# Optimization experiments

Measured on AMD Instinct MI355X. Metric: run time of the kernel, lower is better.

Reference implementation:

```python
import jax, jax.numpy as jnp
import numpy as np
import math


def _conv(x, w, scale, bias, stride=1):
    # Ultralytics-style Conv: Conv2d(bias=False, pad=k//2) + BatchNorm (folded into
    # per-channel scale/bias) + SiLU
    k = w.shape[-1]
    p = k // 2
    y = jax.lax.conv_general_dilated(x, w, (stride, stride), [(p, p), (p, p)],
                                     dimension_numbers=('NCHW', 'OIHW', 'NCHW'))
    y = y * scale[None, :, None, None] + bias[None, :, None, None]
    return y * jax.nn.sigmoid(y)


def setup_inputs() -> dict:
    key = jax.random.key(0)
    ks = jax.random.split(key, 24)
    B, CH1, CH2, H1, W1, HW = 32, 512, 512, 20, 20, 40
    EMB = 256
    s = 0.05
    half = CH1 // 2
    d = {}
    d['x1'] = jax.random.normal(ks[0], (B, CH1, H1, W1), jnp.float32)
    d['x2'] = jax.random.normal(ks[1], (B, CH2, HW, HW), jnp.float32)
    # CrossAttention params
    d['q_w'] = jax.random.normal(ks[2], (EMB, CH1, 3, 3)) * s
    d['q_s'] = 1.0 + jax.random.normal(ks[3], (EMB,)) * s
    d['q_b'] = jax.random.normal(ks[4], (EMB,)) * s
    d['key_w'] = jax.random.normal(ks[5], (EMB, CH2)) * s
    # MGFAB / CSHA params (CA = channel-MLP sigmoid gate, rate=4)
    d['ca_w1'] = jax.random.normal(ks[6], (half // 4, half)) * s
    d['ca_b1'] = jnp.zeros((half // 4,))
    d['ca_w2'] = jax.random.normal(ks[7], (half, half // 4)) * s
    d['ca_b2'] = jnp.zeros((half,))
    d['sa1_w'] = jax.random.normal(ks[8], (half, half, 3, 3)) * s
    d['sa1_s'] = 1.0 + jax.random.normal(ks[9], (half,)) * s
    d['sa1_b'] = jax.random.normal(ks[10], (half,)) * s
    d['sa2_w'] = jax.random.normal(ks[11], (half, half, 3, 3)) * s
    d['sa2_s'] = 1.0 + jax.random.normal(ks[12], (half,)) * s
    d['sa2_b'] = jax.random.normal(ks[13], (half,)) * s
    d['conv2_w'] = jax.random.normal(ks[14], (CH1, 3 * half, 1, 1)) * s
    d['conv2_s'] = 1.0 + jax.random.normal(ks[15], (CH1,)) * s
    d['conv2_b'] = jax.random.normal(ks[16], (CH1,)) * s
    # conv3 branch (single Conv since patch_size[0] < 5)
    d['c3_w'] = jax.random.normal(ks[17], (CH2, CH2, 3, 3)) * s
    d['c3_s'] = 1.0 + jax.random.normal(ks[18], (CH2,)) * s
    d['c3_b'] = jax.random.normal(ks[19], (CH2,)) * s
    return d


def _forward(x1, x2, q_w, q_s, q_b, key_w, ca_w1, ca_b1, ca_w2, ca_b2,
             sa1_w, sa1_s, sa1_b, sa2_w, sa2_s, sa2_b,
             conv2_w, conv2_s, conv2_b, c3_w, c3_s, c3_b):
    NH, PH, PW = 8, 4, 4
    b, c, h, w = x2.shape
    cH = c // NH                       # channels per head
    nph, npw = h // PH, w // PW        # patch grid
    L = nph * npw                      # number of patches == number of q tokens

    # ---- CrossAttention ----
    # value: per-head flattened patches [b*NH, L, cH*PH*PW] (row-major over h,w)
    v = x2.reshape(b * NH, cH, nph, PH, npw, PW).transpose(0, 2, 4, 1, 3, 5)
    v = v.reshape(b * NH, L, cH * PH * PW)
    # key: avg-pool each patch -> linear(c -> emb) -> split heads
    kp = x2.reshape(b, c, nph, PH, npw, PW).mean(axis=(3, 5))  # [b, c, nph, npw]
    k = jnp.einsum('bcl,ec->ble', kp.reshape(b, c, L), key_w)  # [b, L, EMB]
    dh = k.shape[-1] // NH
    k = k.reshape(b, L, NH, dh).transpose(0, 2, 1, 3).reshape(b * NH, L, dh)
    # query: stride-2 conv on x1 -> tokens -> split heads
    q = _conv(x1, q_w, q_s, q_b, stride=2)                     # [b, EMB, nph, npw]
    q = q.reshape(b, -1, L).transpose(0, 2, 1)                 # [b, L, EMB]
    q = q.reshape(b, L, NH, dh).transpose(0, 2, 1, 3).reshape(b * NH, L, dh)
    score = jnp.einsum('nqd,nkd->nqk', q, k) / math.sqrt(dh)
    wts = jax.nn.softmax(score, axis=-1)                       # dropout = identity (eval)
    y = jnp.einsum('nqk,nkv->nqv', wts, v)                     # [b*NH, L, cH*PH*PW]
    # reassemble patches back into [b, c, h, w]
    attn = y.reshape(b, NH, nph, npw, cH, PH, PW).transpose(0, 1, 4, 2, 5, 3, 6)
    attn = attn.reshape(b, c, h, w)

    # ---- conv3 branch with residual ----
    x2_out = _conv(attn, c3_w, c3_s, c3_b) + attn

    x1_up = jnp.repeat(jnp.repeat(x1, 2, axis=2), 2, axis=3)   # [b, ch1, h, w]
    half = x1_up.shape[1] // 2
    a0, a1 = x1_up[:, :half], x1_up[:, half:]
    # CA: channel MLP gate
    xp = a1.transpose(0, 2, 3, 1)                              # [b, h, w, half]
    att = jnp.maximum(xp @ ca_w1.T + ca_b1, 0.0) @ ca_w2.T + ca_b2
    x_ca = a1 * jax.nn.sigmoid(att.transpose(0, 3, 1, 2))
    # SA: two 3x3 Convs + residual
    x_sa = _conv(_conv(x_ca, sa1_w, sa1_s, sa1_b), sa2_w, sa2_s, sa2_b)
    a2 = x_sa + x_ca
    cat = jnp.concatenate([a0, a1, a2], axis=1)                # [b, 3*half, h, w]
    x1_out = _conv(cat, conv2_w, conv2_s, conv2_b)             # [b, ch1, h, w]

    return jnp.concatenate([x1_out, x2_out], axis=1)           # [b, ch1+ch2, h, w]


def reference(x1, x2, q_w, q_s, q_b, key_w, ca_w1, ca_b1, ca_w2, ca_b2,
              sa1_w, sa1_s, sa1_b, sa2_w, sa2_s, sa2_b,
              conv2_w, conv2_s, conv2_b, c3_w, c3_s, c3_b):
    return _forward(x1, x2, q_w, q_s, q_b, key_w, ca_w1, ca_b1, ca_w2, ca_b2,
                    sa1_w, sa1_s, sa1_b, sa2_w, sa2_s, sa2_b,
                    conv2_w, conv2_s, conv2_b, c3_w, c3_s, c3_b)
```

## Files before the change

kernel.cpp:

```cpp
#include <hip/hip_runtime.h>
#include <hip/hip_bf16.h>

using bf16 = __hip_bfloat16;
using bf16x2 = __hip_bfloat162;
typedef __attribute__((ext_vector_type(8))) short short8;
typedef __attribute__((ext_vector_type(4))) float f32x4;

__device__ __forceinline__ float b2f(bf16 v) { return __bfloat162float(v); }
__device__ __forceinline__ bf16 f2b(float v) { return __float2bfloat16(v); }

__device__ __forceinline__ void gload_lds16(const bf16* g, bf16* l)
{
    __builtin_amdgcn_global_load_lds(
        (const __attribute__((address_space(1))) void*)g,
        (__attribute__((address_space(3))) void*)l,
        16, 0, 0);
}

__global__ __launch_bounds__(256) void nchw_to_nhwc(const float* __restrict__ in,
                                                    bf16* __restrict__ out,
                                                    int C, int H, int W, int pad)
{
    __shared__ bf16 tile[64][68];
    const int S = H * W;
    const int HP = H + 2 * pad, WP = W + 2 * pad;
    const int b = blockIdx.x, s0 = blockIdx.y * 64, c0 = blockIdx.z * 64;
    const int t = threadIdx.x;
    const int a = t & 63, q = t >> 6;
#pragma unroll
    for (int i = 0; i < 16; ++i) {
        int cl = q + i * 4;
        int s = s0 + a;
        tile[cl][a] = (s < S) ? f2b(in[((size_t)b * C + c0 + cl) * S + s]) : f2b(0.f);
    }
    __syncthreads();
#pragma unroll
    for (int i = 0; i < 16; ++i) {
        int sl = q + i * 4;
        int s = s0 + sl;
        if (s < S) {
            int y = s / W, x = s - (s / W) * W;
            out[(((size_t)b * HP + y + pad) * WP + x + pad) * C + c0 + a] = tile[a][sl];
        }
    }
}

__global__ __launch_bounds__(256) void halo_zero(bf16* __restrict__ buf, int W, int C)
{
    const int b = blockIdx.x, y = blockIdx.y;
    const int P = W + 2;
    const bf16 z = f2b(0.f);
    bf16* row = buf + ((size_t)b * P + y) * P * C;
    if (y == 0 || y == P - 1) {
        for (int i = threadIdx.x; i < P * C; i += 256) row[i] = z;
    } else {
        for (int i = threadIdx.x; i < 2 * C; i += 256) {
            const int x = (i < C) ? 0 : P - 1;
            const int c = (i < C) ? i : i - C;
            row[(size_t)x * C + c] = z;
        }
    }
}

__global__ __launch_bounds__(256) void pack_out(const bf16* __restrict__ x1o,
                                                const bf16* __restrict__ x2o,
                                                float* __restrict__ out)
{
    __shared__ bf16 tile[64][68];
    const int b = blockIdx.x, s0 = blockIdx.y * 64, ch0 = blockIdx.z * 64;
    const bf16* src = (ch0 < 512) ? x1o : x2o;
    const int c0 = ch0 & 511;
    const int t = threadIdx.x;
    const int a = t & 63, q = t >> 6;
#pragma unroll
    for (int i = 0; i < 16; ++i) {
        int sl = q + i * 4;
        tile[sl][a] = src[((size_t)b * 1600 + s0 + sl) * 512 + c0 + a];
    }
    __syncthreads();
#pragma unroll
    for (int i = 0; i < 16; ++i) {
        int cl = q + i * 4;
        out[((size_t)b * 1024 + ch0 + cl) * 1600 + s0 + a] = b2f(tile[a][cl]);
    }
}

__global__ __launch_bounds__(256) void reorder_w(const float* __restrict__ w,
                                                 bf16* __restrict__ wr,
                                                 int C, int total)
{
    int i = blockIdx.x * 256 + threadIdx.x;
    if (i >= total) return;
    int nineC = 9 * C;
    int o = i / nineC;
    int r = i - o * nineC;
    int tap = r / C;
    int c = r - tap * C;
    wr[i] = f2b(w[((size_t)o * C + c) * 9 + tap]);
}

__global__ __launch_bounds__(256) void f32_to_bf16(const float* __restrict__ in,
                                                   bf16* __restrict__ out, int n)
{
    int i = blockIdx.x * 256 + threadIdx.x;
    if (i < n) out[i] = f2b(in[i]);
}

__global__ __launch_bounds__(256) void pool_kp(const bf16* __restrict__ x2n,
                                               bf16* __restrict__ kp)
{
    const int p = blockIdx.x;
    const int b = p / 100, l = p - (p / 100) * 100;
    const int ph = l / 10, pw = l - (l / 10) * 10;
    const int t = threadIdx.x;
    const bf16x2* base = (const bf16x2*)(x2n + (((size_t)(b * 40 + ph * 4) * 40) + pw * 4) * 512) + t;
    float sx = 0.f, sy = 0.f;
#pragma unroll
    for (int py = 0; py < 4; ++py)
#pragma unroll
        for (int px = 0; px < 4; ++px) {
            float2 v = __bfloat1622float2(base[(py * 40 + px) * 256]);
            sx += v.x; sy += v.y;
        }
    ((bf16x2*)(kp + (size_t)p * 512))[t] = __float22bfloat162_rn(make_float2(sx * 0.0625f, sy * 0.0625f));
}

__global__ __launch_bounds__(256) void ca_mlp(const bf16* __restrict__ x1n,
                                              const float* __restrict__ w1, const float* __restrict__ b1,
                                              const float* __restrict__ w2, const float* __restrict__ b2,
                                              bf16* __restrict__ xca)
{
    __shared__ float a1v[256];
    __shared__ float part[4][64];
    __shared__ float hid[64];
    const int blk = blockIdx.x;
    const int b = blk / 400;
    const int rem = blk - b * 400;
    const int y = rem / 20, x = rem - (rem / 20) * 20;
    const int t = threadIdx.x;
    const bf16* src = x1n + ((size_t)(b * 22 + y + 1) * 22 + x + 1) * 512 + 256;
    a1v[t] = b2f(src[t]);
    __syncthreads();
    {
        const int h = t & 63, seg = t >> 6;
        float acc = 0.f;
        const float* wp = w1 + (size_t)h * 256 + seg * 64;
        const float* ap = a1v + seg * 64;
#pragma unroll 8
        for (int c = 0; c < 64; ++c) acc += wp[c] * ap[c];
        part[seg][h] = acc;
    }
    __syncthreads();
    if (t < 64)
        hid[t] = fmaxf(part[0][t] + part[1][t] + part[2][t] + part[3][t] + b1[t], 0.f);
    __syncthreads();
    float acc2 = b2[t];
    const float* w2p = w2 + (size_t)t * 64;
#pragma unroll 8
    for (int h = 0; h < 64; ++h) acc2 += w2p[h] * hid[h];
    const float g = 1.f / (1.f + __expf(-acc2));
    const bf16 o = f2b(a1v[t] * g);
    const size_t obase = ((size_t)(b * 42 + 2 * y + 1) * 42 + 2 * x + 1) * 256 + t;
    xca[obase] = o;
    xca[obase + 256] = o;
    xca[obase + 42 * 256] = o;
    xca[obase + 42 * 256 + 256] = o;
}

__global__ __launch_bounds__(256, 1)
void attn_kernel(const float* __restrict__ q, const float* __restrict__ k,
                 const bf16* __restrict__ x2n, bf16* __restrict__ attn)
{
    __shared__ float sc[100][100];
    __shared__ bf16 wT[100][104];
    const int t = threadIdx.x;
    const int n = blockIdx.x;
    const int b = n >> 3, hd = n & 7;
    const float* qn = q + (size_t)n * 3200;
    const float* kn = k + (size_t)n * 3200;
    for (int e = t; e < 10000; e += 256) {
        const int i = e / 100;
        const int j = e - i * 100;
        const float4* qa = (const float4*)(qn + i * 32);
        const float4* ka = (const float4*)(kn + j * 32);
        float d = 0.f;
#pragma unroll
        for (int u = 0; u < 8; ++u) {
            float4 xv = qa[u], yv = ka[u];
            d += xv.x * yv.x + xv.y * yv.y + xv.z * yv.z + xv.w * yv.w;
        }
        sc[i][j] = d * 0.17677669529663687f;
    }
    __syncthreads();
    if (t < 100) {
        float mx = -1e30f;
        for (int j = 0; j < 100; ++j) mx = fmaxf(mx, sc[t][j]);
        float s = 0.f;
        for (int j = 0; j < 100; ++j) s += __expf(sc[t][j] - mx);
        const float inv = 1.f / s;
        for (int j = 0; j < 100; ++j) wT[j][t] = f2b(__expf(sc[t][j] - mx) * inv);
    }
    __syncthreads();
    const int ch0 = (t & 15) * 4;
    const int pix = t >> 4;
    const int py = pix >> 2, px = pix & 3;
    const bf16* vbase = x2n + (((size_t)(b * 40 + py) * 40) + px) * 512 + hd * 64 + ch0;
    for (int ql0 = 0; ql0 < 100; ql0 += 20) {
        float2 a0[20], a1[20];
#pragma unroll
        for (int i = 0; i < 20; ++i) { a0[i] = make_float2(0.f, 0.f); a1[i] = make_float2(0.f, 0.f); }
        for (int l = 0; l < 100; ++l) {
            const int ph = l / 10, pw = l - (l / 10) * 10;
            const bf16* vp = vbase + ((size_t)(ph * 160 + pw * 4)) * 512;
            const float2 v01 = __bfloat1622float2(*(const bf16x2*)vp);
            const float2 v23 = __bfloat1622float2(*(const bf16x2*)(vp + 2));
            const bf16x2* wp = (const bf16x2*)&wT[l][ql0];
#pragma unroll
            for (int ii = 0; ii < 10; ++ii) {
                const float2 w2 = __bfloat1622float2(wp[ii]);
                a0[ii * 2 + 0].x += w2.x * v01.x; a0[ii * 2 + 0].y += w2.x * v01.y;
                a1[ii * 2 + 0].x += w2.x * v23.x; a1[ii * 2 + 0].y += w2.x * v23.y;
                a0[ii * 2 + 1].x += w2.y * v01.x; a0[ii * 2 + 1].y += w2.y * v01.y;
                a1[ii * 2 + 1].x += w2.y * v23.x; a1[ii * 2 + 1].y += w2.y * v23.y;
            }
        }
#pragma unroll
        for (int i = 0; i < 20; ++i) {
            const int ql = ql0 + i;
            const int ph = ql / 10, pw = ql - (ql / 10) * 10;
            bf16* op = attn + (((size_t)(b * 42 + ph * 4 + py + 1) * 42) + pw * 4 + px + 1) * 512 + hd * 64 + ch0;
            *(bf16x2*)op = __float22bfloat162_rn(a0[i]);
            *(bf16x2*)(op + 2) = __float22bfloat162_rn(a1[i]);
        }
    }
}

enum ConvMode { M_QCONV = 0, M_SA1 = 1, M_SA2 = 2, M_C3 = 3, M_CONV2 = 4, M_KPROJ = 5 };

template <int MODE>
__global__ __launch_bounds__(256, 2)
void conv_mfma(const bf16* __restrict__ in, const bf16* __restrict__ in2,
               const bf16* __restrict__ wr,
               const float* __restrict__ scale, const float* __restrict__ bias,
               const bf16* __restrict__ resid,
               bf16* __restrict__ outb, float* __restrict__ outf)
{
    constexpr int CIN  = (MODE == M_QCONV || MODE == M_C3 || MODE == M_KPROJ) ? 512
                       : (MODE == M_CONV2 ? 768 : 256);
    constexpr int TAPS = (MODE == M_CONV2 || MODE == M_KPROJ) ? 1 : 9;
    constexpr int SP   = (MODE == M_QCONV || MODE == M_KPROJ) ? 100 : 1600;
    constexpr int STR  = (MODE == M_QCONV) ? 2 : 1;
    constexpr int HP   = (MODE == M_QCONV) ? 22 : 42;
    constexpr int WOUT = (MODE == M_QCONV || MODE == M_KPROJ) ? 10 : 40;
    constexpr int K    = TAPS * CIN;
    constexpr int KD   = (TAPS == 9) ? 3 : 1;

    __shared__ bf16 Al[128][64];
    __shared__ bf16 Bl[128][64];

    const int t = threadIdx.x;
    const int p0 = blockIdx.x * 128;
    const int n0 = blockIdx.y * 128;

    int s_row[4], s_dst8[4], s_src8[4], s_b[4], s_oy[4], s_ox[4];
    const bf16* bB[4];
#pragma unroll
    for (int i = 0; i < 4; ++i) {
        const int task = t + i * 256;
        const int row = task >> 3, chk = task & 7;
        s_row[i] = row;
        s_dst8[i] = chk * 8;
        s_src8[i] = (chk ^ (row & 7)) * 8;
        const int p = p0 + row;
        const int bb = p / SP;
        const int s = p - bb * SP;
        s_b[i] = bb;
        s_oy[i] = s / WOUT;
        s_ox[i] = s - s_oy[i] * WOUT;
        bB[i] = wr + (size_t)(n0 + row) * K + s_src8[i];
    }

    const bf16* aP1[4];
    const bf16* aP2[4];
    if (MODE == M_CONV2) {
#pragma unroll
        for (int i = 0; i < 4; ++i) {
            aP1[i] = in + ((size_t)(s_b[i] * 22 + (s_oy[i] >> 1) + 1) * 22 + (s_ox[i] >> 1) + 1) * 512 + s_src8[i];
            aP2[i] = in2 + ((size_t)(s_b[i] * 1600 + s_oy[i] * 40 + s_ox[i])) * 256 + s_src8[i];
        }
    }
    if (MODE == M_KPROJ) {
#pragma unroll
        for (int i = 0; i < 4; ++i)
            aP1[i] = in + (size_t)(p0 + s_row[i]) * 512 + s_src8[i];
    }

    const int lane = t & 63;
    const int wv = t >> 6;
    const int m_off = (wv >> 1) * 64;
    const int n_off = (wv & 1) * 64;
    const int fr = lane & 15;
    const int qd = lane >> 4;
    const int xa = (fr & 7) << 4;

    f32x4 acc[4][4];
#pragma unroll
    for (int mi = 0; mi < 4; ++mi)
#pragma unroll
        for (int ni = 0; ni < 4; ++ni)
            acc[mi][ni] = (f32x4){0.f, 0.f, 0.f, 0.f};

    for (int ky = 0; ky < KD; ++ky)
    for (int kx = 0; kx < KD; ++kx) {
        const bf16* aT[4];
        if (TAPS == 9) {
#pragma unroll
            for (int i = 0; i < 4; ++i)
                aT[i] = in + ((size_t)((s_b[i] * HP + s_oy[i] * STR + ky) * HP) + s_ox[i] * STR + kx) * CIN + s_src8[i];
        }
        const int kk0 = (ky * KD + kx) * CIN;
        for (int c0 = 0; c0 < CIN; c0 += 64) {
#pragma unroll
            for (int i = 0; i < 4; ++i) {
                const bf16* sa;
                if (MODE == M_CONV2)      sa = (c0 < 512) ? (aP1[i] + c0) : (aP2[i] + (c0 - 512));
                else if (MODE == M_KPROJ) sa = aP1[i] + c0;
                else                      sa = aT[i] + c0;
                gload_lds16(sa, &Al[s_row[i]][s_dst8[i]]);
            }
#pragma unroll
            for (int i = 0; i < 4; ++i)
                gload_lds16(bB[i] + (kk0 + c0), &Bl[s_row[i]][s_dst8[i]]);
            __syncthreads();
#pragma unroll
            for (int ks = 0; ks < 2; ++ks) {
                short8 af[4], bfr[4];
                const int coff = (ks * 64 + qd * 16) ^ xa;
#pragma unroll
                for (int mi = 0; mi < 4; ++mi)
                    af[mi] = *(const short8*)((const char*)&Al[m_off + mi * 16 + fr][0] + coff);
#pragma unroll
                for (int ni = 0; ni < 4; ++ni)
                    bfr[ni] = *(const short8*)((const char*)&Bl[n_off + ni * 16 + fr][0] + coff);
#pragma unroll
                for (int mi = 0; mi < 4; ++mi)
#pragma unroll
                    for (int ni = 0; ni < 4; ++ni)
                        acc[mi][ni] = __builtin_amdgcn_mfma_f32_16x16x32_bf16(af[mi], bfr[ni], acc[mi][ni], 0, 0, 0);
            }
            __syncthreads();
        }
    }

#pragma unroll
    for (int ni = 0; ni < 4; ++ni) {
        const int nn = n0 + n_off + ni * 16 + fr;
        float scv = 1.f, bsv = 0.f;
        if (MODE != M_KPROJ) { scv = scale[nn]; bsv = bias[nn]; }
#pragma unroll
        for (int mi = 0; mi < 4; ++mi) {
            const int mb = p0 + m_off + mi * 16 + qd * 4;
#pragma unroll
            for (int r = 0; r < 4; ++r) {
                const int p = mb + r;
                const float v = acc[mi][ni][r];
                if (MODE == M_KPROJ) {
                    const int bb = p / 100, l = p - (p / 100) * 100;
                    outf[(((size_t)(bb * 8 + (nn >> 5))) * 100 + l) * 32 + (nn & 31)] = v;
                } else {
                    const float y = v * scv + bsv;
                    const float a = y / (1.f + __expf(-y));
                    if (MODE == M_QCONV) {
                        const int bb = p / 100, l = p - (p / 100) * 100;
                        outf[(((size_t)(bb * 8 + (nn >> 5))) * 100 + l) * 32 + (nn & 31)] = a;
                    } else if (MODE == M_SA1) {
                        const int bb = p / 1600; const int s = p - bb * 1600;
                        const int oy = s / 40, ox = s - (s / 40) * 40;
                        outb[(((size_t)(bb * 42 + oy + 1)) * 42 + ox + 1) * 256 + nn] = f2b(a);
                    } else if (MODE == M_SA2) {
                        const int bb = p / 1600; const int s = p - bb * 1600;
                        const int oy = s / 40, ox = s - (s / 40) * 40;
                        const size_t roff = (((size_t)(bb * 42 + oy + 1)) * 42 + ox + 1) * 256 + nn;
                        outb[(size_t)p * 256 + nn] = f2b(a + b2f(resid[roff]));
                    } else if (MODE == M_C3) {
                        const int bb = p / 1600; const int s = p - bb * 1600;
                        const int oy = s / 40, ox = s - (s / 40) * 40;
                        const size_t roff = (((size_t)(bb * 42 + oy + 1)) * 42 + ox + 1) * 512 + nn;
                        outb[(size_t)p * 512 + nn] = f2b(a + b2f(resid[roff]));
                    } else {
                        outb[(size_t)p * 512 + nn] = f2b(a);
                    }
                }
            }
        }
    }
}

extern "C" void kernel_launch(void* const* d_in, const int* in_sizes, int n_in,
                              void* d_out, int out_size, void* d_ws, size_t ws_size,
                              hipStream_t stream)
{
    const float* x1      = (const float*)d_in[0];
    const float* x2      = (const float*)d_in[1];
    const float* q_w     = (const float*)d_in[2];
    const float* q_s     = (const float*)d_in[3];
    const float* q_b     = (const float*)d_in[4];
    const float* key_w   = (const float*)d_in[5];
    const float* ca_w1   = (const float*)d_in[6];
    const float* ca_b1   = (const float*)d_in[7];
    const float* ca_w2   = (const float*)d_in[8];
    const float* ca_b2   = (const float*)d_in[9];
    const float* sa1_w   = (const float*)d_in[10];
    const float* sa1_s   = (const float*)d_in[11];
    const float* sa1_b   = (const float*)d_in[12];
    const float* sa2_w   = (const float*)d_in[13];
    const float* sa2_s   = (const float*)d_in[14];
    const float* sa2_b   = (const float*)d_in[15];
    const float* conv2_w = (const float*)d_in[16];
    const float* conv2_s = (const float*)d_in[17];
    const float* conv2_b = (const float*)d_in[18];
    const float* c3_w    = (const float*)d_in[19];
    const float* c3_s    = (const float*)d_in[20];
    const float* c3_b    = (const float*)d_in[21];

    char* ws = (char*)d_ws;
    const size_t o_x1n  = 0;
    const size_t o_x2n  = 15859712;
    const size_t o_attn = 68288512;
    const size_t o_xca  = 126091264;
    const size_t o_tbuf = 154992640;
    const size_t o_a2   = 183894016;
    const size_t o_ws1  = 210108416;
    const size_t o_ws2  = 211288064;
    const size_t o_wc2  = 212467712;
    const size_t o_k    = o_tbuf;
    const size_t o_q    = o_tbuf + 3276800;
    const size_t o_wkey = o_tbuf + 6553600;
    const size_t o_kp   = o_a2;
    const size_t o_wq   = o_a2 + 3276800;
    const size_t o_wc3  = o_xca;

    bf16*  x1n    = (bf16*)(ws + o_x1n);
    bf16*  x2n    = (bf16*)(ws + o_x2n);
    float* k_attn = (float*)(ws + o_k);
    float* q_attn = (float*)(ws + o_q);
    bf16*  attn   = (bf16*)(ws + o_attn);
    bf16*  xca    = (bf16*)(ws + o_xca);
    bf16*  tbuf   = (bf16*)(ws + o_tbuf);
    bf16*  a2     = (bf16*)(ws + o_a2);
    bf16*  wq     = (bf16*)(ws + o_wq);
    bf16*  wc3    = (bf16*)(ws + o_wc3);
    bf16*  wsa1   = (bf16*)(ws + o_ws1);
    bf16*  wsa2   = (bf16*)(ws + o_ws2);
    bf16*  kp     = (bf16*)(ws + o_kp);
    bf16*  wkey   = (bf16*)(ws + o_wkey);
    bf16*  wc2    = (bf16*)(ws + o_wc2);
    bf16*  x2o    = (bf16*)(ws + o_x2n);
    bf16*  x1o    = (bf16*)(ws + o_attn);

    const dim3 blk(256);

    halo_zero<<<dim3(32, 22), blk, 0, stream>>>(x1n, 20, 512);
    halo_zero<<<dim3(32, 42), blk, 0, stream>>>(xca, 40, 256);
    halo_zero<<<dim3(32, 42), blk, 0, stream>>>(attn, 40, 512);

    nchw_to_nhwc<<<dim3(32, 7, 8), blk, 0, stream>>>(x1, x1n, 512, 20, 20, 1);
    nchw_to_nhwc<<<dim3(32, 25, 8), blk, 0, stream>>>(x2, x2n, 512, 40, 40, 0);
    reorder_w<<<4608, blk, 0, stream>>>(q_w,  wq,   512, 256 * 512 * 9);
    reorder_w<<<2304, blk, 0, stream>>>(sa1_w, wsa1, 256, 256 * 256 * 9);
    reorder_w<<<2304, blk, 0, stream>>>(sa2_w, wsa2, 256, 256 * 256 * 9);
    f32_to_bf16<<<512, blk, 0, stream>>>(key_w, wkey, 256 * 512);
    f32_to_bf16<<<1536, blk, 0, stream>>>(conv2_w, wc2, 512 * 768);
    pool_kp<<<3200, blk, 0, stream>>>(x2n, kp);

    conv_mfma<M_KPROJ><<<dim3(25, 2), blk, 0, stream>>>(kp, nullptr, wkey,
        nullptr, nullptr, nullptr, nullptr, k_attn);
    conv_mfma<M_QCONV><<<dim3(25, 2), blk, 0, stream>>>(x1n, nullptr, wq,
        q_s, q_b, nullptr, nullptr, q_attn);

    attn_kernel<<<256, blk, 0, stream>>>(q_attn, k_attn, x2n, attn);

    halo_zero<<<dim3(32, 42), blk, 0, stream>>>(tbuf, 40, 256);

    ca_mlp<<<12800, blk, 0, stream>>>(x1n, ca_w1, ca_b1, ca_w2, ca_b2, xca);

    conv_mfma<M_SA1><<<dim3(400, 2), blk, 0, stream>>>(xca, nullptr, wsa1,
        sa1_s, sa1_b, nullptr, tbuf, nullptr);
    conv_mfma<M_SA2><<<dim3(400, 2), blk, 0, stream>>>(tbuf, nullptr, wsa2,
        sa2_s, sa2_b, xca, a2, nullptr);

    reorder_w<<<9216, blk, 0, stream>>>(c3_w, wc3, 512, 512 * 512 * 9);
    conv_mfma<M_C3><<<dim3(400, 4), blk, 0, stream>>>(attn, nullptr, wc3,
        c3_s, c3_b, attn, x2o, nullptr);
    conv_mfma<M_CONV2><<<dim3(400, 4), blk, 0, stream>>>(x1n, a2, wc2,
        conv2_s, conv2_b, nullptr, x1o, nullptr);

    pack_out<<<dim3(32, 25, 16), blk, 0, stream>>>(x1o, x2o, (float*)d_out);

    (void)in_sizes; (void)n_in; (void)out_size; (void)ws_size;
}
```

Before: 1.464 ms.

## Add double-buffered 256x256-tile MFMA conv kernel for large convolutions

Adds a new 512-thread implicit-GEMM conv kernel with 256x256 output tiles and double-buffered LDS. It prefetches the next K-slice with direct global-to-LDS loads interleaved between MFMA phases, using explicit barriers and s_setprio. The SA1, SA2, C3 and CONV2 convolutions now use it, and the old kernel is trimmed to the small Q-conv and key-projection cases. Larger tiles raise operand reuse and the overlap hides load latency, but LDS use grows to 128KB per block. The SA convs now launch only 200 blocks, which may underfill the GPU.

```diff
diff --git a/kernel.cpp b/kernel.cpp
--- a/kernel.cpp
+++ b/kernel.cpp
@@ -16,6 +16,10 @@
         (__attribute__((address_space(3))) void*)l,
         16, 0, 0);
 }
+
+#define PH_BAR() do { __builtin_amdgcn_sched_barrier(0); __builtin_amdgcn_s_barrier(); __builtin_amdgcn_sched_barrier(0); } while (0)
+#define WAIT_LGKM0() do { asm volatile("s_waitcnt lgkmcnt(0)" ::: "memory"); __builtin_amdgcn_sched_barrier(0); } while (0)
+#define WAIT_VM0() do { asm volatile("s_waitcnt vmcnt(0)" ::: "memory"); __builtin_amdgcn_sched_barrier(0); } while (0)
 
 __global__ __launch_bounds__(256) void nchw_to_nhwc(const float* __restrict__ in,
                                                     bf16* __restrict__ out,
@@ -239,19 +243,15 @@
 
 template <int MODE>
 __global__ __launch_bounds__(256, 2)
-void conv_mfma(const bf16* __restrict__ in, const bf16* __restrict__ in2,
-               const bf16* __restrict__ wr,
+void conv_mfma(const bf16* __restrict__ in, const bf16* __restrict__ wr,
                const float* __restrict__ scale, const float* __restrict__ bias,
-               const bf16* __restrict__ resid,
-               bf16* __restrict__ outb, float* __restrict__ outf)
-{
-    constexpr int CIN  = (MODE == M_QCONV || MODE == M_C3 || MODE == M_KPROJ) ? 512
-                       : (MODE == M_CONV2 ? 768 : 256);
-    constexpr int TAPS = (MODE == M_CONV2 || MODE == M_KPROJ) ? 1 : 9;
-    constexpr int SP   = (MODE == M_QCONV || MODE == M_KPROJ) ? 100 : 1600;
-    constexpr int STR  = (MODE == M_QCONV) ? 2 : 1;
-    constexpr int HP   = (MODE == M_QCONV) ? 22 : 42;
-    constexpr int WOUT = (MODE == M_QCONV || MODE == M_KPROJ) ? 10 : 40;
+               float* __restrict__ outf)
+{
+    constexpr int CIN  = 512;
+    constexpr int TAPS = (MODE == M_KPROJ) ? 1 : 9;
+    constexpr int STR  = 2;
+    constexpr int HP   = 22;
+    constexpr int WOUT = 10;
     constexpr int K    = TAPS * CIN;
     constexpr int KD   = (TAPS == 9) ? 3 : 1;
 
@@ -272,8 +272,8 @@
         s_dst8[i] = chk * 8;
         s_src8[i] = (chk ^ (row & 7)) * 8;
         const int p = p0 + row;
-        const int bb = p / SP;
-        const int s = p - bb * SP;
+        const int bb = p / 100;
+        const int s = p - bb * 100;
         s_b[i] = bb;
         s_oy[i] = s / WOUT;
         s_ox[i] = s - s_oy[i] * WOUT;
@@ -281,14 +281,6 @@
     }
 
     const bf16* aP1[4];
-    const bf16* aP2[4];
-    if (MODE == M_CONV2) {
-#pragma unroll
-        for (int i = 0; i < 4; ++i) {
-            aP1[i] = in + ((size_t)(s_b[i] * 22 + (s_oy[i] >> 1) + 1) * 22 + (s_ox[i] >> 1) + 1) * 512 + s_src8[i];
-            aP2[i] = in2 + ((size_t)(s_b[i] * 1600 + s_oy[i] * 40 + s_ox[i])) * 256 + s_src8[i];
-        }
-    }
     if (MODE == M_KPROJ) {
 #pragma unroll
         for (int i = 0; i < 4; ++i)
@@ -322,10 +314,7 @@
         for (int c0 = 0; c0 < CIN; c0 += 64) {
 #pragma unroll
             for (int i = 0; i < 4; ++i) {
-                const bf16* sa;
-                if (MODE == M_CONV2)      sa = (c0 < 512) ? (aP1[i] + c0) : (aP2[i] + (c0 - 512));
-                else if (MODE == M_KPROJ) sa = aP1[i] + c0;
-                else                      sa = aT[i] + c0;
+                const bf16* sa = (MODE == M_KPROJ) ? (aP1[i] + c0) : (aT[i] + c0);
                 gload_lds16(sa, &Al[s_row[i]][s_dst8[i]]);
             }
 #pragma unroll
@@ -364,32 +353,235 @@
             for (int r = 0; r < 4; ++r) {
                 const int p = mb + r;
                 const float v = acc[mi][ni][r];
+                const int bb = p / 100, l = p - (p / 100) * 100;
                 if (MODE == M_KPROJ) {
-                    const int bb = p / 100, l = p - (p / 100) * 100;
                     outf[(((size_t)(bb * 8 + (nn >> 5))) * 100 + l) * 32 + (nn & 31)] = v;
                 } else {
                     const float y = v * scv + bsv;
                     const float a = y / (1.f + __expf(-y));
-                    if (MODE == M_QCONV) {
-                        const int bb = p / 100, l = p - (p / 100) * 100;
-                        outf[(((size_t)(bb * 8 + (nn >> 5))) * 100 + l) * 32 + (nn & 31)] = a;
-                    } else if (MODE == M_SA1) {
-                        const int bb = p / 1600; const int s = p - bb * 1600;
-                        const int oy = s / 40, ox = s - (s / 40) * 40;
-                        outb[(((size_t)(bb * 42 + oy + 1)) * 42 + ox + 1) * 256 + nn] = f2b(a);
-                    } else if (MODE == M_SA2) {
-                        const int bb = p / 1600; const int s = p - bb * 1600;
-                        const int oy = s / 40, ox = s - (s / 40) * 40;
-                        const size_t roff = (((size_t)(bb * 42 + oy + 1)) * 42 + ox + 1) * 256 + nn;
-                        outb[(size_t)p * 256 + nn] = f2b(a + b2f(resid[roff]));
-                    } else if (MODE == M_C3) {
-                        const int bb = p / 1600; const int s = p - bb * 1600;
-                        const int oy = s / 40, ox = s - (s / 40) * 40;
-                        const size_t roff = (((size_t)(bb * 42 + oy + 1)) * 42 + ox + 1) * 512 + nn;
-                        outb[(size_t)p * 512 + nn] = f2b(a + b2f(resid[roff]));
-                    } else {
-                        outb[(size_t)p * 512 + nn] = f2b(a);
-                    }
+                    outf[(((size_t)(bb * 8 + (nn >> 5))) * 100 + l) * 32 + (nn & 31)] = a;
+                }
+            }
+        }
+    }
+}
+
+template <int MODE>
+__global__ __launch_bounds__(512, 2)
+void conv_mfma256(const bf16* __restrict__ in, const bf16* __restrict__ in2,
+                  const bf16* __restrict__ wr,
+                  const float* __restrict__ scale, const float* __restrict__ bias,
+                  const bf16* __restrict__ resid,
+                  bf16* __restrict__ outb)
+{
+    constexpr int CIN  = (MODE == M_C3) ? 512 : (MODE == M_CONV2 ? 768 : 256);
+    constexpr int TAPS = (MODE == M_CONV2) ? 1 : 9;
+    constexpr int K    = TAPS * CIN;
+    constexpr int NT   = K / 64;
+    constexpr int CPT  = CIN / 64;
+    constexpr int L2C  = (CPT == 8) ? 3 : 2;
+    constexpr int HP   = 42;
+
+    __shared__ bf16 Al[2][256][64];
+    __shared__ bf16 Bl[2][256][64];
+
+    const int t = threadIdx.x;
+    const int p0 = blockIdx.x * 256;
+    const int n0 = blockIdx.y * 256;
+
+    const int row64 = t >> 3;
+    const int chk = t & 7;
+    const int src8 = (chk ^ (row64 & 7)) * 8;
+    const int dst8 = chk * 8;
+
+    const bf16* aBase[4];
+    const bf16* aBase2[4];
+#pragma unroll
+    for (int si = 0; si < 4; ++si) {
+        const int p = p0 + si * 64 + row64;
+        const int b = p / 1600;
+        const int s = p - b * 1600;
+        const int oy = s / 40, ox = s - (s / 40) * 40;
+        if (MODE == M_CONV2) {
+            aBase[si]  = in  + ((size_t)(b * 22 + (oy >> 1) + 1) * 22 + (ox >> 1) + 1) * 512 + src8;
+            aBase2[si] = in2 + ((size_t)(b * 1600 + oy * 40 + ox)) * 256 + src8;
+        } else {
+            aBase[si]  = in  + ((size_t)(b * HP + oy) * HP + ox) * CIN + src8;
+            aBase2[si] = nullptr;
+        }
+    }
+    const bf16* bBase[4];
+#pragma unroll
+    for (int si = 0; si < 4; ++si)
+        bBase[si] = wr + (size_t)(n0 + si * 64 + row64) * K + src8;
+
+    const int lane = t & 63;
+    const int wv = t >> 6;
+    const int m_off = (wv >> 2) * 128;
+    const int n_off = (wv & 3) * 64;
+    const int fr = lane & 15;
+    const int qd = lane >> 4;
+    const int xa = (fr & 7) << 4;
+
+    f32x4 acc[8][4];
+#pragma unroll
+    for (int mi = 0; mi < 8; ++mi)
+#pragma unroll
+        for (int ni = 0; ni < 4; ++ni)
+            acc[mi][ni] = (f32x4){0.f, 0.f, 0.f, 0.f};
+
+#define LDA8(buf, rrow, kkk) \
+    (*(const short8*)((const char*)&Al[buf][rrow][0] + ((((kkk) * 64) + qd * 16) ^ xa)))
+#define LDB8(buf, rrow, kkk) \
+    (*(const short8*)((const char*)&Bl[buf][rrow][0] + ((((kkk) * 64) + qd * 16) ^ xa)))
+
+#pragma unroll
+    for (int si = 0; si < 4; ++si)
+        gload_lds16(aBase[si], &Al[0][si * 64 + row64][dst8]);
+#pragma unroll
+    for (int si = 0; si < 4; ++si)
+        gload_lds16(bBase[si], &Bl[0][si * 64 + row64][dst8]);
+    asm volatile("s_waitcnt vmcnt(0)" ::: "memory");
+    __syncthreads();
+
+#pragma clang loop unroll(disable)
+    for (int kt = 0; kt < NT; ++kt) {
+        const int cur = kt & 1;
+        const int nxt = cur ^ 1;
+        const int ktn = kt + 1;
+        const bool pf = (ktn < NT);
+        int offAn = 0, c0n = 0;
+        if (pf) {
+            if (MODE == M_CONV2) {
+                c0n = ktn * 64;
+            } else {
+                const int tap = ktn >> L2C;
+                const int ci = ktn & (CPT - 1);
+                const int ky = tap / 3, kx = tap - ky * 3;
+                offAn = (ky * HP + kx) * CIN + ci * 64;
+            }
+        }
+        const int offBn = ktn * 64;
+
+        auto stage = [&](int si) {
+            if (si < 4) {
+                const bf16* sa;
+                if (MODE == M_CONV2) sa = (c0n < 512) ? (aBase[si] + c0n) : (aBase2[si] + (c0n - 512));
+                else sa = aBase[si] + offAn;
+                gload_lds16(sa, &Al[nxt][si * 64 + row64][dst8]);
+            } else {
+                gload_lds16(bBase[si - 4] + offBn, &Bl[nxt][(si - 4) * 64 + row64][dst8]);
+            }
+        };
+
+        short8 af[4][2], bf0[2][2], bf1[2][2];
+
+#pragma unroll
+        for (int m4 = 0; m4 < 4; ++m4) {
+            af[m4][0] = LDA8(cur, m_off + m4 * 16 + fr, 0);
+            af[m4][1] = LDA8(cur, m_off + m4 * 16 + fr, 1);
+        }
+#pragma unroll
+        for (int n2 = 0; n2 < 2; ++n2) {
+            bf0[n2][0] = LDB8(cur, n_off + n2 * 16 + fr, 0);
+            bf0[n2][1] = LDB8(cur, n_off + n2 * 16 + fr, 1);
+        }
+        if (pf) { stage(0); stage(1); stage(2); }
+        PH_BAR();
+        WAIT_LGKM0();
+        __builtin_amdgcn_s_setprio(1);
+#pragma unroll
+        for (int m4 = 0; m4 < 4; ++m4)
+#pragma unroll
+            for (int n2 = 0; n2 < 2; ++n2) {
+                acc[m4][n2] = __builtin_amdgcn_mfma_f32_16x16x32_bf16(af[m4][0], bf0[n2][0], acc[m4][n2], 0, 0, 0);
+                acc[m4][n2] = __builtin_amdgcn_mfma_f32_16x16x32_bf16(af[m4][1], bf0[n2][1], acc[m4][n2], 0, 0, 0);
+            }
+        __builtin_amdgcn_s_setprio(0);
+        PH_BAR();
+
+#pragma unroll
+        for (int n2 = 0; n2 < 2; ++n2) {
+            bf1[n2][0] = LDB8(cur, n_off + (2 + n2) * 16 + fr, 0);
+            bf1[n2][1] = LDB8(cur, n_off + (2 + n2) * 16 + fr, 1);
+        }
+        if (pf) { stage(3); stage(4); stage(5); }
+        PH_BAR();
+        WAIT_LGKM0();
+        __builtin_amdgcn_s_setprio(1);
+#pragma unroll
+        for (int m4 = 0; m4 < 4; ++m4)
+#pragma unroll
+            for (int n2 = 0; n2 < 2; ++n2) {
+                acc[m4][2 + n2] = __builtin_amdgcn_mfma_f32_16x16x32_bf16(af[m4][0], bf1[n2][0], acc[m4][2 + n2], 0, 0, 0);
+                acc[m4][2 + n2] = __builtin_amdgcn_mfma_f32_16x16x32_bf16(af[m4][1], bf1[n2][1], acc[m4][2 + n2], 0, 0, 0);
+            }
+        __builtin_amdgcn_s_setprio(0);
+        PH_BAR();
+
+#pragma unroll
+        for (int m4 = 0; m4 < 4; ++m4) {
+            af[m4][0] = LDA8(cur, m_off + (4 + m4) * 16 + fr, 0);
+            af[m4][1] = LDA8(cur, m_off + (4 + m4) * 16 + fr, 1);
+        }
+        if (pf) { stage(6); stage(7); }
+        PH_BAR();
+        WAIT_LGKM0();
+        __builtin_amdgcn_s_setprio(1);
+#pragma unroll
+        for (int m4 = 0; m4 < 4; ++m4)
+#pragma unroll
+            for (int n2 = 0; n2 < 2; ++n2) {
+                acc[4 + m4][n2] = __builtin_amdgcn_mfma_f32_16x16x32_bf16(af[m4][0], bf0[n2][0], acc[4 + m4][n2], 0, 0, 0);
+                acc[4 + m4][n2] = __builtin_amdgcn_mfma_f32_16x16x32_bf16(af[m4][1], bf0[n2][1], acc[4 + m4][n2], 0, 0, 0);
+            }
+        __builtin_amdgcn_s_setprio(0);
+        PH_BAR();
+
+        __builtin_amdgcn_s_setprio(1);
+#pragma unroll
+        for (int m4 = 0; m4 < 4; ++m4)
+#pragma unroll
+            for (int n2 = 0; n2 < 2; ++n2) {
+                acc[4 + m4][2 + n2] = __builtin_amdgcn_mfma_f32_16x16x32_bf16(af[m4][0], bf1[n2][0], acc[4 + m4][2 + n2], 0, 0, 0);
+                acc[4 + m4][2 + n2] = __builtin_amdgcn_mfma_f32_16x16x32_bf16(af[m4][1], bf1[n2][1], acc[4 + m4][2 + n2], 0, 0, 0);
+            }
+        __builtin_amdgcn_s_setprio(0);
+        WAIT_VM0();
+        PH_BAR();
+    }
+#undef LDA8
+#undef LDB8
+
+#pragma unroll
+    for (int ni = 0; ni < 4; ++ni) {
+        const int nn = n0 + n_off + ni * 16 + fr;
+        const float scv = scale[nn];
+        const float bsv = bias[nn];
+#pragma unroll
+        for (int mi = 0; mi < 8; ++mi) {
+            const int mb = p0 + m_off + mi * 16 + qd * 4;
+#pragma unroll
+            for (int r = 0; r < 4; ++r) {
+                const int p = mb + r;
+                const float y = acc[mi][ni][r] * scv + bsv;
+                const float a = y / (1.f + __expf(-y));
+                if (MODE == M_SA1) {
+                    const int bb = p / 1600; const int s = p - bb * 1600;
+                    const int oy = s / 40, ox = s - (s / 40) * 40;
+                    outb[(((size_t)(bb * 42 + oy + 1)) * 42 + ox + 1) * 256 + nn] = f2b(a);
+                } else if (MODE == M_SA2) {
+                    const int bb = p / 1600; const int s = p - bb * 1600;
+                    const int oy = s / 40, ox = s - (s / 40) * 40;
+                    const size_t roff = (((size_t)(bb * 42 + oy + 1)) * 42 + ox + 1) * 256 + nn;
+                    outb[(size_t)p * 256 + nn] = f2b(a + b2f(resid[roff]));
+                } else if (MODE == M_C3) {
+                    const int bb = p / 1600; const int s = p - bb * 1600;
+                    const int oy = s / 40, ox = s - (s / 40) * 40;
+                    const size_t roff = (((size_t)(bb * 42 + oy + 1)) * 42 + ox + 1) * 512 + nn;
+                    outb[(size_t)p * 512 + nn] = f2b(a + b2f(resid[roff]));
+                } else {
+                    outb[(size_t)p * 512 + nn] = f2b(a);
                 }
             }
         }
@@ -459,6 +651,7 @@
     bf16*  x1o    = (bf16*)(ws + o_attn);
 
     const dim3 blk(256);
+    const dim3 blk512(512);
 
     halo_zero<<<dim3(32, 22), blk, 0, stream>>>(x1n, 20, 512);
     halo_zero<<<dim3(32, 42), blk, 0, stream>>>(xca, 40, 256);
@@ -473,10 +666,8 @@
     f32_to_bf16<<<1536, blk, 0, stream>>>(conv2_w, wc2, 512 * 768);
     pool_kp<<<3200, blk, 0, stream>>>(x2n, kp);
 
-    conv_mfma<M_KPROJ><<<dim3(25, 2), blk, 0, stream>>>(kp, nullptr, wkey,
-        nullptr, nullptr, nullptr, nullptr, k_attn);
-    conv_mfma<M_QCONV><<<dim3(25, 2), blk, 0, stream>>>(x1n, nullptr, wq,
-        q_s, q_b, nullptr, nullptr, q_attn);
+    conv_mfma<M_KPROJ><<<dim3(25, 2), blk, 0, stream>>>(kp, wkey, nullptr, nullptr, k_attn);
+    conv_mfma<M_QCONV><<<dim3(25, 2), blk, 0, stream>>>(x1n, wq, q_s, q_b, q_attn);
 
     attn_kernel<<<256, blk, 0, stream>>>(q_attn, k_attn, x2n, attn);
 
@@ -484,16 +675,16 @@
 
     ca_mlp<<<12800, blk, 0, stream>>>(x1n, ca_w1, ca_b1, ca_w2, ca_b2, xca);
 
-    conv_mfma<M_SA1><<<dim3(400, 2), blk, 0, stream>>>(xca, nullptr, wsa1,
-        sa1_s, sa1_b, nullptr, tbuf, nullptr);
-    conv_mfma<M_SA2><<<dim3(400, 2), blk, 0, stream>>>(tbuf, nullptr, wsa2,
-        sa2_s, sa2_b, xca, a2, nullptr);
+    conv_mfma256<M_SA1><<<dim3(200, 1), blk512, 0, stream>>>(xca, nullptr, wsa1,
+        sa1_s, sa1_b, nullptr, tbuf);
+    conv_mfma256<M_SA2><<<dim3(200, 1), blk512, 0, stream>>>(tbuf, nullptr, wsa2,
+        sa2_s, sa2_b, xca, a2);
 
     reorder_w<<<9216, blk, 0, stream>>>(c3_w, wc3, 512, 512 * 512 * 9);
-    conv_mfma<M_C3><<<dim3(400, 4), blk, 0, stream>>>(attn, nullptr, wc3,
-        c3_s, c3_b, attn, x2o, nullptr);
-    conv_mfma<M_CONV2><<<dim3(400, 4), blk, 0, stream>>>(x1n, a2, wc2,
-        conv2_s, conv2_b, nullptr, x1o, nullptr);
+    conv_mfma256<M_C3><<<dim3(200, 2), blk512, 0, stream>>>(attn, nullptr, wc3,
+        c3_s, c3_b, attn, x2o);
+    conv_mfma256<M_CONV2><<<dim3(200, 2), blk512, 0, stream>>>(x1n, a2, wc2,
+        conv2_s, conv2_b, nullptr, x1o);
 
     pack_out<<<dim3(32, 25, 16), blk, 0, stream>>>(x1o, x2o, (float*)d_out);
 
```

After: 1.473 ms. Within noise of the previous version (+0.6%).
